# Kernel tuning notes

Measured on AMD Instinct MI355X. Metric: run time of the kernel, lower is better.

## Reference

```python
import jax, jax.numpy as jnp
import numpy as np

D = 16      # stroke_embedding_dim
H = 2       # num_heads
DH = D // H # head dim = 8
HID = 32    # hidden_dim
OUT = 32    # output_dim
N = 250000  # num edge nodes
F = 500000  # num faces
E = 4       # edges per face


def setup_inputs() -> dict:
    key = jax.random.key(0)
    ks = jax.random.split(key, 10)
    s = 1.0 / np.sqrt(D)
    return {
        "node_embed": jax.random.normal(ks[0], (1, N, D), dtype=jnp.float32),
        "face_edge_ids": jax.random.randint(ks[1], (F, E), 0, N),
        # nn.MultiheadAttention in_proj (packed q,k,v) and out_proj, stored [in, out]
        "w_in": jax.random.uniform(ks[2], (D, 3 * D), jnp.float32, -s, s),
        "b_in": jnp.zeros((3 * D,), jnp.float32),
        "w_out": jax.random.uniform(ks[3], (D, D), jnp.float32, -s, s),
        "b_out": jnp.zeros((D,), jnp.float32),
        # fc: Linear(16 -> 32), fc_output: Linear(32 -> 32)
        "fc_w": jax.random.uniform(ks[4], (D, HID), jnp.float32, -s, s),
        "fc_b": jax.random.uniform(ks[5], (HID,), jnp.float32, -s, s),
        "fco_w": jax.random.uniform(ks[6], (HID, OUT), jnp.float32, -1 / np.sqrt(HID), 1 / np.sqrt(HID)),
        "fco_b": jax.random.uniform(ks[7], (OUT,), jnp.float32, -1 / np.sqrt(HID), 1 / np.sqrt(HID)),
    }


def reference(node_embed, face_edge_ids, w_in, b_in, w_out, b_out, fc_w, fc_b, fco_w, fco_b):
    # Gather per-face edge embeddings: [F, E, D]
    x = node_embed[0][face_edge_ids]
    # Packed qkv projection
    qkv = x @ w_in + b_in                                  # [F, E, 3D]
    q, k, v = jnp.split(qkv, 3, axis=-1)
    def heads(t):
        return t.reshape(F, E, H, DH).transpose(0, 2, 1, 3)  # [F, H, E, DH]
    q, k, v = heads(q), heads(k), heads(v)
    scores = jnp.einsum("fhqd,fhkd->fhqk", q, k) / np.sqrt(DH)
    attn = jax.nn.softmax(scores, axis=-1)
    o = jnp.einsum("fhqk,fhkd->fhqd", attn, v)             # [F, H, E, DH]
    o = o.transpose(0, 2, 1, 3).reshape(F, E, D)
    attn_out = o @ w_out + b_out                           # [F, E, D]
    h = jax.nn.relu(attn_out @ fc_w + fc_b)                # [F, E, HID]
    pooled = h.mean(axis=1)                                # [F, HID]
    out = pooled @ fco_w + fco_b                           # [F, OUT]
    return out[None]                                       # [1, F, OUT]
```

## Files before the change

### kernel.cpp

```cpp
#include <hip/hip_runtime.h>
#include <stdint.h>


typedef _Float16 v2h __attribute__((ext_vector_type(2)));
typedef __fp16 h4 __attribute__((ext_vector_type(4)));
typedef float f32x4 __attribute__((ext_vector_type(4)));
typedef uint32_t u32x2 __attribute__((ext_vector_type(2)));

#define DPP_ROT1 0x39
#define DPP_ROT2 0x4E
#define DPP_ROT3 0x93

template<int CTRL>
static __device__ __forceinline__ float dppf(float x) {
    return __builtin_bit_cast(float,
        __builtin_amdgcn_mov_dpp(__builtin_bit_cast(int, x), CTRL, 0xF, 0xF, true));
}

static __device__ __forceinline__ v2h pkh(float a, float b) {
    v2h r; r.x = (_Float16)a; r.y = (_Float16)b; return r;
}
static __device__ __forceinline__ v2h pkrtz(float a, float b) {
#if __has_builtin(__builtin_amdgcn_cvt_pkrtz)
    return __builtin_bit_cast(v2h, __builtin_amdgcn_cvt_pkrtz(a, b));
#else
    return pkh(a, b);
#endif
}
static __device__ __forceinline__ uint32_t bcu(v2h h) {
    return __builtin_bit_cast(uint32_t, h);
}
static __device__ __forceinline__ h4 mkh4(uint32_t lo, uint32_t hi) {
    u32x2 t; t.x = lo; t.y = hi; return __builtin_bit_cast(h4, t);
}
static __device__ __forceinline__ h4 ld2h(const uint32_t* p) {
    u32x2 t; t.x = p[0]; t.y = p[1]; return __builtin_bit_cast(h4, t);
}
static __device__ __forceinline__ f32x4 mfma16(h4 a, h4 b, f32x4 c) {
    return __builtin_amdgcn_mfma_f32_16x16x16f16(a, b, c, 0, 0, 0);
}
static __device__ __forceinline__ h4 packC(f32x4 c) {
    return mkh4(bcu(pkrtz(c[0], c[1])), bcu(pkrtz(c[2], c[3])));
}
static __device__ __forceinline__ h4 packCrelu(f32x4 c) {
    return mkh4(bcu(pkrtz(fmaxf(c[0], 0.f), fmaxf(c[1], 0.f))),
                bcu(pkrtz(fmaxf(c[2], 0.f), fmaxf(c[3], 0.f))));
}
static __device__ __forceinline__ h4 selh(bool keep, h4 x) {
    u32x2 t = __builtin_bit_cast(u32x2, x);
    u32x2 r; r.x = keep ? t.x : 0u; r.y = keep ? t.y : 0u;
    return __builtin_bit_cast(h4, r);
}

__global__ void fold_w(const float* __restrict__ w_in,
                       const float* __restrict__ w_out,
                       const float* __restrict__ b_out,
                       const float* __restrict__ fc_w,
                       const float* __restrict__ fc_b,
                       const float* __restrict__ fco_w,
                       uint32_t* __restrict__ wsu) {
    const int tid = threadIdx.x;
    if (blockIdx.x == 0) {
        if (tid < 384) {
            const int T = tid >> 7, r = tid & 127, l = r >> 1, d = r & 1;
            const int o = 16 * T + (l & 15), k0 = 4 * (l >> 4) + 2 * d;
            wsu[tid] = bcu(pkh(w_in[k0 * 48 + o], w_in[(k0 + 1) * 48 + o]));
        } else if (tid < 640) {
            const int i = tid - 384, b = i >> 7, r = i & 127, l = r >> 1, d = r & 1;
            const int c = 16 * b + (l & 15), k0 = 4 * (l >> 4) + 2 * d;
            float a0 = 0.f, a1 = 0.f;
#pragma unroll
            for (int e = 0; e < 16; ++e) {
                a0 = fmaf(w_out[k0 * 16 + e],       fc_w[e * 32 + c], a0);
                a1 = fmaf(w_out[(k0 + 1) * 16 + e], fc_w[e * 32 + c], a1);
            }
            wsu[tid] = bcu(pkh(a0, a1));
        }
    } else {
        if (tid < 32) {
            float acc = fc_b[tid];
#pragma unroll
            for (int e = 0; e < 16; ++e)
                acc = fmaf(b_out[e], fc_w[e * 32 + tid], acc);
            reinterpret_cast<float*>(wsu)[640 + tid] = acc;
        } else if (tid < 544) {
            const int i = tid - 32;
            const int kt = i >> 8, n = (i >> 7) & 1, r = i & 127, l = r >> 1, d = r & 1;
            const int col = 16 * n + (l & 15), k0 = 16 * kt + 4 * (l >> 4) + 2 * d;
            wsu[672 + i] = bcu(pkh(fco_w[k0 * 32 + col] * 0.25f,
                                   fco_w[(k0 + 1) * 32 + col] * 0.25f));
        }
    }
}

__global__ void cvt_node(const float* __restrict__ node,
                         uint32_t* __restrict__ nt, int ndw) {
    const int i = blockIdx.x * 256 + threadIdx.x;
    if (i < ndw) nt[i] = bcu(pkrtz(node[2 * i], node[2 * i + 1]));
}

template<bool F16>
__launch_bounds__(256, 6)
__global__ void face_net(const float* __restrict__ node,
                         const uint32_t* __restrict__ nt,
                         const int*   __restrict__ fids,
                         const float* __restrict__ b_in,
                         const uint32_t* __restrict__ wsu,
                         const float* __restrict__ fco_b,
                         float* __restrict__ out, int F) {
    const int l   = threadIdx.x & 63;
    const int wid = threadIdx.x >> 6;
    const int token_base = blockIdx.x * 256 + wid * 64;
    const int total = 4 * F;
    if (token_base >= total) return;
    const int c0 = l & 15, g2 = l >> 4;

    h4 X[4];
#pragma unroll
    for (int a = 0; a < 4; ++a) {
        int tok = token_base + 16 * a + c0;
        tok = tok < total ? tok : total - 1;
        const int nid = fids[tok];
        if constexpr (F16) {
            const u32x2 xw = *reinterpret_cast<const u32x2*>(
                nt + (size_t)nid * 8 + g2 * 2);
            X[a] = __builtin_bit_cast(h4, xw);
        } else {
            const float4 xv = *reinterpret_cast<const float4*>(
                node + (size_t)nid * 16 + g2 * 4);
            X[a] = mkh4(bcu(pkrtz(xv.x, xv.y)), bcu(pkrtz(xv.z, xv.w)));
        }
    }

    const h4 WqT  = ld2h(wsu + 0   + l * 2);
    const h4 WkT  = ld2h(wsu + 128 + l * 2);
    const h4 WvB  = ld2h(wsu + 256 + l * 2);
    const h4 EhA0 = ld2h(wsu + 384 + l * 2);
    const h4 EhA1 = ld2h(wsu + 512 + l * 2);
    const h4 Ef00 = ld2h(wsu + 672 + 0 * 128 + l * 2);
    const h4 Ef01 = ld2h(wsu + 672 + 1 * 128 + l * 2);
    const h4 Ef10 = ld2h(wsu + 672 + 2 * 128 + l * 2);
    const h4 Ef11 = ld2h(wsu + 672 + 3 * 128 + l * 2);

    const float4 bq4 = *reinterpret_cast<const float4*>(b_in + 4 * g2);
    const float  bv  = b_in[32 + c0];
    const float* b1f = reinterpret_cast<const float*>(wsu) + 640;
    const float4 b10 = *reinterpret_cast<const float4*>(b1f + 4 * g2);
    const float4 b11 = *reinterpret_cast<const float4*>(b1f + 16 + 4 * g2);
    const float fb0s = fco_b[c0];
    const float fb1s = fco_b[16 + c0];

    const bool scoreH0 = (g2 < 2);
    const bool pvH0    = (c0 < 8);
    const bool valid   = (g2 == (c0 >> 2));
    const int fbase = token_base >> 2;
    const float C = 0.51006974841f;
    const f32x4 zz = {0.f, 0.f, 0.f, 0.f};
    const f32x4 cq = {bq4.x, bq4.y, bq4.z, bq4.w};
    const f32x4 cv = {bv, bv, bv, bv};
    const f32x4 ch0 = {b10.x, b10.y, b10.z, b10.w};
    const f32x4 ch1 = {b11.x, b11.y, b11.z, b11.w};

#pragma unroll
    for (int ap = 0; ap < 2; ++ap) {
        f32x4 Dq[2], Dk[2], Dv[2];
#pragma unroll
        for (int j = 0; j < 2; ++j) {
            const h4 x = X[2 * ap + j];
            Dq[j] = mfma16(WqT, x, cq);
            Dk[j] = mfma16(WkT, x, zz);
            Dv[j] = mfma16(x, WvB, cv);
        }
        h4 qB[2], kA[2], vA[2];
#pragma unroll
        for (int j = 0; j < 2; ++j) {
            qB[j] = packC(Dq[j]); kA[j] = packC(Dk[j]); vA[j] = packC(Dv[j]);
        }
        f32x4 S0[2], S1[2];
#pragma unroll
        for (int j = 0; j < 2; ++j) {
            S0[j] = mfma16(selh(scoreH0,  kA[j]), qB[j], zz);
            S1[j] = mfma16(selh(!scoreH0, kA[j]), qB[j], zz);
        }
        h4 PB0[2], PB1[2];
#pragma unroll
        for (int j = 0; j < 2; ++j) {
            const float e00 = __builtin_amdgcn_exp2f(S0[j][0] * C);
            const float e01 = __builtin_amdgcn_exp2f(S0[j][1] * C);
            const float e02 = __builtin_amdgcn_exp2f(S0[j][2] * C);
            const float e03 = __builtin_amdgcn_exp2f(S0[j][3] * C);
            const float e10 = __builtin_amdgcn_exp2f(S1[j][0] * C);
            const float e11 = __builtin_amdgcn_exp2f(S1[j][1] * C);
            const float e12 = __builtin_amdgcn_exp2f(S1[j][2] * C);
            const float e13 = __builtin_amdgcn_exp2f(S1[j][3] * C);
            const float r0 = __builtin_amdgcn_rcpf((e00 + e01) + (e02 + e03));
            const float r1 = __builtin_amdgcn_rcpf((e10 + e11) + (e12 + e13));
            PB0[j] = selh(valid, mkh4(bcu(pkrtz(e00 * r0, e01 * r0)),
                                      bcu(pkrtz(e02 * r0, e03 * r0))));
            PB1[j] = selh(valid, mkh4(bcu(pkrtz(e10 * r1, e11 * r1)),
                                      bcu(pkrtz(e12 * r1, e13 * r1))));
        }
        f32x4 Ot[2];
#pragma unroll
        for (int j = 0; j < 2; ++j) {
            Ot[j] = mfma16(selh(pvH0,  vA[j]), PB0[j], zz);
            Ot[j] = mfma16(selh(!pvH0, vA[j]), PB1[j], Ot[j]);
        }
        h4 hB[2];
#pragma unroll
        for (int j = 0; j < 2; ++j) hB[j] = packC(Ot[j]);
        f32x4 H0[2], H1[2];
#pragma unroll
        for (int j = 0; j < 2; ++j) {
            H0[j] = mfma16(EhA0, hB[j], ch0);
            H1[j] = mfma16(EhA1, hB[j], ch1);
        }
        f32x4 O0[2], O1[2];
#pragma unroll
        for (int j = 0; j < 2; ++j) {
            const h4 AH0 = packCrelu(H0[j]);
            const h4 AH1 = packCrelu(H1[j]);
            O0[j] = mfma16(AH1, Ef10, mfma16(AH0, Ef00, zz));
            O1[j] = mfma16(AH1, Ef11, mfma16(AH0, Ef01, zz));
        }
#pragma unroll
        for (int j = 0; j < 2; ++j) {
            const int a = 2 * ap + j;
            const float o0 = ((O0[j][0] + O0[j][1]) + (O0[j][2] + O0[j][3])) + fb0s;
            const float o1 = ((O1[j][0] + O1[j][1]) + (O1[j][2] + O1[j][3])) + fb1s;
            const float a1 = dppf<DPP_ROT1>(o0);
            const float a2 = dppf<DPP_ROT2>(o0);
            const float a3 = dppf<DPP_ROT3>(o0);
            const float b1 = dppf<DPP_ROT1>(o1);
            const float b2 = dppf<DPP_ROT2>(o1);
            const float b3 = dppf<DPP_ROT3>(o1);
            const int face = fbase + 4 * a + g2;
            if ((c0 & 2) == 0 && face < F) {
                const bool t0 = (c0 & 1) == 0;
                const int q = c0 >> 2;
                const float4 st = make_float4(t0 ? o0 : b3,
                                              t0 ? a1 : o1,
                                              t0 ? a2 : b1,
                                              t0 ? a3 : b2);
                float* ob = out + (size_t)face * 32 + (t0 ? 4 * q : 16 + 4 * q);
                *reinterpret_cast<float4*>(ob) = st;
            }
        }
    }
}

extern "C" void kernel_launch(void* const* d_in, const int* in_sizes, int n_in,
                              void* d_out, int out_size, void* d_ws, size_t ws_size,
                              hipStream_t stream) {
    const float* node  = (const float*)d_in[0];
    const int*   fids  = (const int*)  d_in[1];
    const float* w_in  = (const float*)d_in[2];
    const float* b_in  = (const float*)d_in[3];
    const float* w_out = (const float*)d_in[4];
    const float* b_out = (const float*)d_in[5];
    const float* fc_w  = (const float*)d_in[6];
    const float* fc_b  = (const float*)d_in[7];
    const float* fco_w = (const float*)d_in[8];
    const float* fco_b = (const float*)d_in[9];
    float* out = (float*)d_out;
    uint32_t* wsu = (uint32_t*)d_ws;
    const int F = in_sizes[1] / 4;
    const int ndw = in_sizes[0] / 2;
    const size_t need = (2048 + (size_t)ndw) * 4;
    const bool f16tab = ws_size >= need;

    hipLaunchKernelGGL(fold_w, dim3(2), dim3(640), 0, stream,
                       w_in, w_out, b_out, fc_w, fc_b, fco_w, wsu);
    if (f16tab) {
        hipLaunchKernelGGL(cvt_node, dim3((ndw + 255) / 256), dim3(256), 0,
                           stream, node, wsu + 2048, ndw);
    }
    const int threads = F * 4;
    const int blocks = (threads + 255) / 256;
    if (f16tab) {
        hipLaunchKernelGGL((face_net<true>), dim3(blocks), dim3(256), 0, stream,
                           node, wsu + 2048, fids, b_in, wsu, fco_b, out, F);
    } else {
        hipLaunchKernelGGL((face_net<false>), dim3(blocks), dim3(256), 0, stream,
                           node, wsu, fids, b_in, wsu, fco_b, out, F);
    }
}
```

Baseline: 134.5 us.

## Make face_net persistent grid-stride with software-prefetched gathers

Caps the grid at 2048 blocks and turns each wave into a grid-stride loop that issues the next tile's index and node gathers before computing the current tile. The aim is to hide gather latency behind the MFMA chain and to amortise the per-wave weight and bias loads over several tiles. In exchange it adds live registers for the prefetched tile, which could cut occupancy under the 6-wave launch bound, and a fixed grid size may leave CUs unevenly loaded.

```diff
diff --git a/kernel.cpp b/kernel.cpp
--- a/kernel.cpp
+++ b/kernel.cpp
@@ -100,25 +100,14 @@
 }
 
 template<bool F16>
-__launch_bounds__(256, 6)
-__global__ void face_net(const float* __restrict__ node,
-                         const uint32_t* __restrict__ nt,
-                         const int*   __restrict__ fids,
-                         const float* __restrict__ b_in,
-                         const uint32_t* __restrict__ wsu,
-                         const float* __restrict__ fco_b,
-                         float* __restrict__ out, int F) {
-    const int l   = threadIdx.x & 63;
-    const int wid = threadIdx.x >> 6;
-    const int token_base = blockIdx.x * 256 + wid * 64;
-    const int total = 4 * F;
-    if (token_base >= total) return;
-    const int c0 = l & 15, g2 = l >> 4;
-
-    h4 X[4];
+static __device__ __forceinline__ void gather4(h4* X,
+                                               const float* __restrict__ node,
+                                               const uint32_t* __restrict__ nt,
+                                               const int* __restrict__ fids,
+                                               int tb, int total, int c0, int g2) {
 #pragma unroll
     for (int a = 0; a < 4; ++a) {
-        int tok = token_base + 16 * a + c0;
+        int tok = tb + 16 * a + c0;
         tok = tok < total ? tok : total - 1;
         const int nid = fids[tok];
         if constexpr (F16) {
@@ -131,6 +120,24 @@
             X[a] = mkh4(bcu(pkrtz(xv.x, xv.y)), bcu(pkrtz(xv.z, xv.w)));
         }
     }
+}
+
+template<bool F16>
+__launch_bounds__(256, 6)
+__global__ void face_net(const float* __restrict__ node,
+                         const uint32_t* __restrict__ nt,
+                         const int*   __restrict__ fids,
+                         const float* __restrict__ b_in,
+                         const uint32_t* __restrict__ wsu,
+                         const float* __restrict__ fco_b,
+                         float* __restrict__ out, int F) {
+    const int l   = threadIdx.x & 63;
+    const int wid = threadIdx.x >> 6;
+    const int total = 4 * F;
+    const int c0 = l & 15, g2 = l >> 4;
+    int tb = (blockIdx.x * 4 + wid) * 64;
+    if (tb >= total) return;
+    const int stride = gridDim.x * 256;
 
     const h4 WqT  = ld2h(wsu + 0   + l * 2);
     const h4 WkT  = ld2h(wsu + 128 + l * 2);
@@ -153,7 +160,6 @@
     const bool scoreH0 = (g2 < 2);
     const bool pvH0    = (c0 < 8);
     const bool valid   = (g2 == (c0 >> 2));
-    const int fbase = token_base >> 2;
     const float C = 0.51006974841f;
     const f32x4 zz = {0.f, 0.f, 0.f, 0.f};
     const f32x4 cq = {bq4.x, bq4.y, bq4.z, bq4.w};
@@ -161,91 +167,105 @@
     const f32x4 ch0 = {b10.x, b10.y, b10.z, b10.w};
     const f32x4 ch1 = {b11.x, b11.y, b11.z, b11.w};
 
-#pragma unroll
-    for (int ap = 0; ap < 2; ++ap) {
-        f32x4 Dq[2], Dk[2], Dv[2];
-#pragma unroll
-        for (int j = 0; j < 2; ++j) {
-            const h4 x = X[2 * ap + j];
-            Dq[j] = mfma16(WqT, x, cq);
-            Dk[j] = mfma16(WkT, x, zz);
-            Dv[j] = mfma16(x, WvB, cv);
+    h4 X[4];
+    gather4<F16>(X, node, nt, fids, tb, total, c0, g2);
+
+    for (; tb < total; tb += stride) {
+        h4 Xn[4];
+        const int tbn = tb + stride;
+        if (tbn < total)
+            gather4<F16>(Xn, node, nt, fids, tbn, total, c0, g2);
+
+        const int fbase = tb >> 2;
+#pragma unroll
+        for (int ap = 0; ap < 2; ++ap) {
+            f32x4 Dq[2], Dk[2], Dv[2];
+#pragma unroll
+            for (int j = 0; j < 2; ++j) {
+                const h4 x = X[2 * ap + j];
+                Dq[j] = mfma16(WqT, x, cq);
+                Dk[j] = mfma16(WkT, x, zz);
+                Dv[j] = mfma16(x, WvB, cv);
+            }
+            h4 qB[2], kA[2], vA[2];
+#pragma unroll
+            for (int j = 0; j < 2; ++j) {
+                qB[j] = packC(Dq[j]); kA[j] = packC(Dk[j]); vA[j] = packC(Dv[j]);
+            }
+            f32x4 S0[2], S1[2];
+#pragma unroll
+            for (int j = 0; j < 2; ++j) {
+                S0[j] = mfma16(selh(scoreH0,  kA[j]), qB[j], zz);
+                S1[j] = mfma16(selh(!scoreH0, kA[j]), qB[j], zz);
+            }
+            h4 PB0[2], PB1[2];
+#pragma unroll
+            for (int j = 0; j < 2; ++j) {
+                const float e00 = __builtin_amdgcn_exp2f(S0[j][0] * C);
+                const float e01 = __builtin_amdgcn_exp2f(S0[j][1] * C);
+                const float e02 = __builtin_amdgcn_exp2f(S0[j][2] * C);
+                const float e03 = __builtin_amdgcn_exp2f(S0[j][3] * C);
+                const float e10 = __builtin_amdgcn_exp2f(S1[j][0] * C);
+                const float e11 = __builtin_amdgcn_exp2f(S1[j][1] * C);
+                const float e12 = __builtin_amdgcn_exp2f(S1[j][2] * C);
+                const float e13 = __builtin_amdgcn_exp2f(S1[j][3] * C);
+                const float r0 = __builtin_amdgcn_rcpf((e00 + e01) + (e02 + e03));
+                const float r1 = __builtin_amdgcn_rcpf((e10 + e11) + (e12 + e13));
+                PB0[j] = selh(valid, mkh4(bcu(pkrtz(e00 * r0, e01 * r0)),
+                                          bcu(pkrtz(e02 * r0, e03 * r0))));
+                PB1[j] = selh(valid, mkh4(bcu(pkrtz(e10 * r1, e11 * r1)),
+                                          bcu(pkrtz(e12 * r1, e13 * r1))));
+            }
+            f32x4 Ot[2];
+#pragma unroll
+            for (int j = 0; j < 2; ++j) {
+                Ot[j] = mfma16(selh(pvH0,  vA[j]), PB0[j], zz);
+                Ot[j] = mfma16(selh(!pvH0, vA[j]), PB1[j], Ot[j]);
+            }
+            h4 hB[2];
+#pragma unroll
+            for (int j = 0; j < 2; ++j) hB[j] = packC(Ot[j]);
+            f32x4 H0[2], H1[2];
+#pragma unroll
+            for (int j = 0; j < 2; ++j) {
+                H0[j] = mfma16(EhA0, hB[j], ch0);
+                H1[j] = mfma16(EhA1, hB[j], ch1);
+            }
+            f32x4 O0[2], O1[2];
+#pragma unroll
+            for (int j = 0; j < 2; ++j) {
+                const h4 AH0 = packCrelu(H0[j]);
+                const h4 AH1 = packCrelu(H1[j]);
+                O0[j] = mfma16(AH1, Ef10, mfma16(AH0, Ef00, zz));
+                O1[j] = mfma16(AH1, Ef11, mfma16(AH0, Ef01, zz));
+            }
+#pragma unroll
+            for (int j = 0; j < 2; ++j) {
+                const int a = 2 * ap + j;
+                const float o0 = ((O0[j][0] + O0[j][1]) + (O0[j][2] + O0[j][3])) + fb0s;
+                const float o1 = ((O1[j][0] + O1[j][1]) + (O1[j][2] + O1[j][3])) + fb1s;
+                const float a1 = dppf<DPP_ROT1>(o0);
+                const float a2 = dppf<DPP_ROT2>(o0);
+                const float a3 = dppf<DPP_ROT3>(o0);
+                const float b1 = dppf<DPP_ROT1>(o1);
+                const float b2 = dppf<DPP_ROT2>(o1);
+                const float b3 = dppf<DPP_ROT3>(o1);
+                const int face = fbase + 4 * a + g2;
+                if ((c0 & 2) == 0 && face < F) {
+                    const bool t0 = (c0 & 1) == 0;
+                    const int q = c0 >> 2;
+                    const float4 st = make_float4(t0 ? o0 : b3,
+                                                  t0 ? a1 : o1,
+                                                  t0 ? a2 : b1,
+                                                  t0 ? a3 : b2);
+                    float* ob = out + (size_t)face * 32 + (t0 ? 4 * q : 16 + 4 * q);
+                    *reinterpret_cast<float4*>(ob) = st;
+                }
+            }
         }
-        h4 qB[2], kA[2], vA[2];
-#pragma unroll
-        for (int j = 0; j < 2; ++j) {
-            qB[j] = packC(Dq[j]); kA[j] = packC(Dk[j]); vA[j] = packC(Dv[j]);
-        }
-        f32x4 S0[2], S1[2];
-#pragma unroll
-        for (int j = 0; j < 2; ++j) {
-            S0[j] = mfma16(selh(scoreH0,  kA[j]), qB[j], zz);
-            S1[j] = mfma16(selh(!scoreH0, kA[j]), qB[j], zz);
-        }
-        h4 PB0[2], PB1[2];
-#pragma unroll
-        for (int j = 0; j < 2; ++j) {
-            const float e00 = __builtin_amdgcn_exp2f(S0[j][0] * C);
-            const float e01 = __builtin_amdgcn_exp2f(S0[j][1] * C);
-            const float e02 = __builtin_amdgcn_exp2f(S0[j][2] * C);
-            const float e03 = __builtin_amdgcn_exp2f(S0[j][3] * C);
-            const float e10 = __builtin_amdgcn_exp2f(S1[j][0] * C);
-            const float e11 = __builtin_amdgcn_exp2f(S1[j][1] * C);
-            const float e12 = __builtin_amdgcn_exp2f(S1[j][2] * C);
-            const float e13 = __builtin_amdgcn_exp2f(S1[j][3] * C);
-            const float r0 = __builtin_amdgcn_rcpf((e00 + e01) + (e02 + e03));
-            const float r1 = __builtin_amdgcn_rcpf((e10 + e11) + (e12 + e13));
-            PB0[j] = selh(valid, mkh4(bcu(pkrtz(e00 * r0, e01 * r0)),
-                                      bcu(pkrtz(e02 * r0, e03 * r0))));
-            PB1[j] = selh(valid, mkh4(bcu(pkrtz(e10 * r1, e11 * r1)),
-                                      bcu(pkrtz(e12 * r1, e13 * r1))));
-        }
-        f32x4 Ot[2];
-#pragma unroll
-        for (int j = 0; j < 2; ++j) {
-            Ot[j] = mfma16(selh(pvH0,  vA[j]), PB0[j], zz);
-            Ot[j] = mfma16(selh(!pvH0, vA[j]), PB1[j], Ot[j]);
-        }
-        h4 hB[2];
-#pragma unroll
-        for (int j = 0; j < 2; ++j) hB[j] = packC(Ot[j]);
-        f32x4 H0[2], H1[2];
-#pragma unroll
-        for (int j = 0; j < 2; ++j) {
-            H0[j] = mfma16(EhA0, hB[j], ch0);
-            H1[j] = mfma16(EhA1, hB[j], ch1);
-        }
-        f32x4 O0[2], O1[2];
-#pragma unroll
-        for (int j = 0; j < 2; ++j) {
-            const h4 AH0 = packCrelu(H0[j]);
-            const h4 AH1 = packCrelu(H1[j]);
-            O0[j] = mfma16(AH1, Ef10, mfma16(AH0, Ef00, zz));
-            O1[j] = mfma16(AH1, Ef11, mfma16(AH0, Ef01, zz));
-        }
-#pragma unroll
-        for (int j = 0; j < 2; ++j) {
-            const int a = 2 * ap + j;
-            const float o0 = ((O0[j][0] + O0[j][1]) + (O0[j][2] + O0[j][3])) + fb0s;
-            const float o1 = ((O1[j][0] + O1[j][1]) + (O1[j][2] + O1[j][3])) + fb1s;
-            const float a1 = dppf<DPP_ROT1>(o0);
-            const float a2 = dppf<DPP_ROT2>(o0);
-            const float a3 = dppf<DPP_ROT3>(o0);
-            const float b1 = dppf<DPP_ROT1>(o1);
-            const float b2 = dppf<DPP_ROT2>(o1);
-            const float b3 = dppf<DPP_ROT3>(o1);
-            const int face = fbase + 4 * a + g2;
-            if ((c0 & 2) == 0 && face < F) {
-                const bool t0 = (c0 & 1) == 0;
-                const int q = c0 >> 2;
-                const float4 st = make_float4(t0 ? o0 : b3,
-                                              t0 ? a1 : o1,
-                                              t0 ? a2 : b1,
-                                              t0 ? a3 : b2);
-                float* ob = out + (size_t)face * 32 + (t0 ? 4 * q : 16 + 4 * q);
-                *reinterpret_cast<float4*>(ob) = st;
-            }
-        }
+
+#pragma unroll
+        for (int a = 0; a < 4; ++a) X[a] = Xn[a];
     }
 }
 
@@ -275,8 +295,9 @@
         hipLaunchKernelGGL(cvt_node, dim3((ndw + 255) / 256), dim3(256), 0,
                            stream, node, wsu + 2048, ndw);
     }
-    const int threads = F * 4;
-    const int blocks = (threads + 255) / 256;
+    const int total = F * 4;
+    const int blocks_needed = (total + 255) / 256;
+    const int blocks = blocks_needed < 2048 ? blocks_needed : 2048;
     if (f16tab) {
         hipLaunchKernelGGL((face_net<true>), dim3(blocks), dim3(256), 0, stream,
                            node, wsu + 2048, fids, b_in, wsu, fco_b, out, F);
```

Result: slower. 143.6 us (+6.7%).
